# Performance work log

Measured on AMD Instinct MI355X. Metric: run time of the kernel, lower is better.

## Reference

```python
import jax, jax.numpy as jnp
import numpy as np

N_EMBD = 1024
N_HEAD = 16
B, T = 1, 4096
EPS = 1e-5


def layer_norm(x, w):
    mu = jnp.mean(x, axis=-1, keepdims=True)
    var = jnp.var(x, axis=-1, keepdims=True)
    return (x - mu) / jnp.sqrt(var + EPS) * w


def setup_inputs() -> dict:
    key = jax.random.key(0)
    ks = jax.random.split(key, 6)
    s = 0.02
    return {
        "x": jax.random.normal(ks[0], (B, T, N_EMBD), dtype=jnp.float32),
        "w_qkv": jax.random.normal(ks[1], (N_EMBD, 3 * N_EMBD), dtype=jnp.float32) * s,
        "w_attn_proj": jax.random.normal(ks[2], (N_EMBD, N_EMBD), dtype=jnp.float32) * s,
        "w_fc": jax.random.normal(ks[3], (N_EMBD, 4 * N_EMBD), dtype=jnp.float32) * s,
        "w_mlp_proj": jax.random.normal(ks[4], (4 * N_EMBD, N_EMBD), dtype=jnp.float32) * s,
        "ln1_w": jnp.ones((N_EMBD,), dtype=jnp.float32),
        "ln2_w": jnp.ones((N_EMBD,), dtype=jnp.float32),
    }


def reference(x, w_qkv, w_attn_proj, w_fc, w_mlp_proj, ln1_w, ln2_w):
    Bq, Tq, C = x.shape
    hs = C // N_HEAD

    # --- attention branch (pre-norm) ---
    h = layer_norm(x, ln1_w)
    qkv = h @ w_qkv  # [B,T,3C]
    q, k, v = jnp.split(qkv, 3, axis=-1)
    q = q.reshape(Bq, Tq, N_HEAD, hs).transpose(0, 2, 1, 3)  # [B,H,T,hs]
    k = k.reshape(Bq, Tq, N_HEAD, hs).transpose(0, 2, 1, 3)
    v = v.reshape(Bq, Tq, N_HEAD, hs).transpose(0, 2, 1, 3)

    scores = jnp.einsum("bhqd,bhkd->bhqk", q, k) * (1.0 / jnp.sqrt(jnp.float32(hs)))
    causal = jnp.tril(jnp.ones((Tq, Tq), dtype=bool))
    scores = jnp.where(causal, scores, -jnp.inf)
    weights = jax.nn.softmax(scores, axis=-1)  # dropout=0 -> identity
    out = jnp.einsum("bhqk,bhkd->bhqd", weights, v)
    out = out.transpose(0, 2, 1, 3).reshape(Bq, Tq, C)
    x = x + out @ w_attn_proj

    # --- MLP branch (pre-norm) ---
    h = layer_norm(x, ln2_w)
    h = jax.nn.gelu(h @ w_fc, approximate=False)  # nn.GELU default is exact
    x = x + h @ w_mlp_proj
    return x
```

## Files before the change

kernel.cpp:

```cpp
#include <hip/hip_runtime.h>
#include <cstdint>

typedef __attribute__((ext_vector_type(8))) short short8;
typedef __attribute__((ext_vector_type(4))) float f32x4;

__device__ __forceinline__ float b2f(unsigned short u) {
    return __uint_as_float(((unsigned int)u) << 16);
}
__device__ __forceinline__ unsigned short f2b(float f) {
    unsigned int u = __float_as_uint(f);
    u += 0x7FFFu + ((u >> 16) & 1u);
    return (unsigned short)(u >> 16);
}

__device__ __forceinline__ void gload_lds16(const unsigned short* g, unsigned short* l) {
    __builtin_amdgcn_global_load_lds(
        (const __attribute__((address_space(1))) uint32_t*)g,
        (__attribute__((address_space(3))) uint32_t*)l, 16, 0, 0);
}

__global__ __launch_bounds__(256) void k_transpose_bf16(
        const float* __restrict__ w, unsigned short* __restrict__ wT, int K, int N) {
    __shared__ float tile[32][33];
    int n0 = blockIdx.x * 32, k0 = blockIdx.y * 32;
    int tx = threadIdx.x, ty = threadIdx.y;
#pragma unroll
    for (int i = 0; i < 4; i++)
        tile[ty + 8 * i][tx] = w[(size_t)(k0 + ty + 8 * i) * N + n0 + tx];
    __syncthreads();
#pragma unroll
    for (int i = 0; i < 4; i++)
        wT[(size_t)(n0 + ty + 8 * i) * K + k0 + tx] = f2b(tile[tx][ty + 8 * i]);
}

__global__ __launch_bounds__(256) void k_layernorm(
        const float* __restrict__ x, const float* __restrict__ w,
        unsigned short* __restrict__ out) {
    int row = blockIdx.x, tid = threadIdx.x;
    const float4* xr = (const float4*)(x + (size_t)row * 1024);
    float4 v = xr[tid];
    float s  = v.x + v.y + v.z + v.w;
    float ss = v.x * v.x + v.y * v.y + v.z * v.z + v.w * v.w;
#pragma unroll
    for (int off = 32; off >= 1; off >>= 1) {
        s  += __shfl_down(s, off);
        ss += __shfl_down(ss, off);
    }
    __shared__ float red[10];
    if ((tid & 63) == 0) { red[tid >> 6] = s; red[4 + (tid >> 6)] = ss; }
    __syncthreads();
    if (tid == 0) {
        float S  = red[0] + red[1] + red[2] + red[3];
        float SS = red[4] + red[5] + red[6] + red[7];
        float mu  = S * (1.0f / 1024.0f);
        float var = SS * (1.0f / 1024.0f) - mu * mu;
        red[8] = mu; red[9] = rsqrtf(var + 1e-5f);
    }
    __syncthreads();
    float mu = red[8], rs = red[9];
    float4 wv = ((const float4*)w)[tid];
    ushort4 pk;
    pk.x = f2b((v.x - mu) * rs * wv.x);
    pk.y = f2b((v.y - mu) * rs * wv.y);
    pk.z = f2b((v.z - mu) * rs * wv.z);
    pk.w = f2b((v.w - mu) * rs * wv.w);
    *(ushort4*)(out + (size_t)row * 1024 + tid * 4) = pk;
}

template <int EPI, int TN>
__global__ __launch_bounds__(256) void k_gemm_bt(
        const unsigned short* __restrict__ A, const unsigned short* __restrict__ BT,
        const float* __restrict__ RES, void* __restrict__ OUT,
        int M, int N, int K) {
    constexpr int MI = (TN == 128) ? 4 : 2;
    __shared__ __align__(16) unsigned short As[128 * 64];
    __shared__ __align__(16) unsigned short Bs[TN * 64];
    int tid  = threadIdx.x;
    int lane = tid & 63, wave = tid >> 6;
    int quad = lane >> 4, qr = lane & 15;
    int wm_off = (TN == 128) ? (wave >> 1) * 64 : wave * 32;
    int wn_off = (TN == 128) ? (wave & 1) * 64 : 0;
    int m0 = blockIdx.y * 128, n0 = blockIdx.x * TN;
    int lrow = lane >> 3;
    int gcol = 8 * (((lane & 7) - lrow) & 7);
    int cswz[2];
#pragma unroll
    for (int kk = 0; kk < 2; kk++) cswz[kk] = 8 * (((kk * 4) + quad + (qr & 7)) & 7);
    f32x4 acc[MI][4] = {};
    for (int k0 = 0; k0 < K; k0 += 64) {
        __syncthreads();
#pragma unroll
        for (int t = 0; t < 4; t++) {
            int rowb = wave * 32 + t * 8;
            gload_lds16(&A[(size_t)(m0 + rowb + lrow) * K + k0 + gcol], &As[rowb * 64]);
        }
#pragma unroll
        for (int t = 0; t < TN / 32; t++) {
            int rowb = wave * (TN / 4) + t * 8;
            gload_lds16(&BT[(size_t)(n0 + rowb + lrow) * K + k0 + gcol], &Bs[rowb * 64]);
        }
        __syncthreads();
#pragma unroll
        for (int kk = 0; kk < 2; kk++) {
            short8 af[MI], bfr[4];
#pragma unroll
            for (int i = 0; i < MI; i++) af[i]  = *(const short8*)&As[(wm_off + i * 16 + qr) * 64 + cswz[kk]];
#pragma unroll
            for (int j = 0; j < 4; j++)  bfr[j] = *(const short8*)&Bs[(wn_off + j * 16 + qr) * 64 + cswz[kk]];
#pragma unroll
            for (int i = 0; i < MI; i++)
#pragma unroll
                for (int j = 0; j < 4; j++)
                    acc[i][j] = __builtin_amdgcn_mfma_f32_16x16x32_bf16(af[i], bfr[j], acc[i][j], 0, 0, 0);
        }
    }
#pragma unroll
    for (int i = 0; i < MI; i++) {
#pragma unroll
        for (int j = 0; j < 4; j++) {
#pragma unroll
            for (int r = 0; r < 4; r++) {
                int row = m0 + wm_off + i * 16 + quad * 4 + r;
                int col = n0 + wn_off + j * 16 + qr;
                size_t idx = (size_t)row * N + col;
                float v = acc[i][j][r];
                if (EPI == 0)      ((float*)OUT)[idx] = v;
                else if (EPI == 1) ((unsigned short*)OUT)[idx] = f2b(v);
                else if (EPI == 2) ((float*)OUT)[idx] = RES[idx] + v;
                else {
                    float u = v * fmaf(v * v, 0.035677408f, 0.79788456f);
                    float e = fminf(u * 2.885390082f, 80.0f);
                    float t = exp2f(e);
                    float g = v * t / (t + 1.0f);
                    ((unsigned short*)OUT)[idx] = f2b(g);
                }
            }
        }
    }
}

__global__ __launch_bounds__(256) void k_attn(
        const unsigned short* __restrict__ qkv, unsigned short* __restrict__ out) {
    __shared__ unsigned short Ks[128][72];
    __shared__ unsigned short Vt[64][136];
    __shared__ unsigned short Ps[4][16][136];

    const float C1 = 0.18033688f;
    const float C2 = 5.77078016f;

    int l = blockIdx.x;
    int h = l & 15;
    int qb = 63 - (l >> 4);
    int q0 = qb * 64;

    int tid = threadIdx.x;
    int wave = tid >> 6, lane = tid & 63;
    int lane16 = lane & 15, quad = lane >> 4;

    {
        int srow = tid >> 2, sc0 = (tid & 3) * 16;
        size_t base = (size_t)(q0 + srow) * 3072 + h * 64 + sc0;
        *(uint4*)&Ks[srow][sc0]     = *(const uint4*)&qkv[base];
        *(uint4*)&Ks[srow][sc0 + 8] = *(const uint4*)&qkv[base + 8];
    }
    __syncthreads();
    short8 aq0 = *(const short8*)&Ks[wave * 16 + lane16][quad * 8];
    short8 aq1 = *(const short8*)&Ks[wave * 16 + lane16][32 + quad * 8];

    f32x4 Oacc[4] = {};
    float l_part[4] = {0.f, 0.f, 0.f, 0.f};

    int vk = (lane & 31) * 2;
    int d0 = wave * 16 + (lane >> 5) * 8;

    for (int kc = 0; kc <= qb; kc += 2) {
        __syncthreads();
        {
            int srow = tid >> 1, c0 = (tid & 1) * 32;
            size_t base = (size_t)(kc * 64 + srow) * 3072 + 1024 + h * 64 + c0;
            *(uint4*)&Ks[srow][c0]      = *(const uint4*)&qkv[base];
            *(uint4*)&Ks[srow][c0 + 8]  = *(const uint4*)&qkv[base + 8];
            *(uint4*)&Ks[srow][c0 + 16] = *(const uint4*)&qkv[base + 16];
            *(uint4*)&Ks[srow][c0 + 24] = *(const uint4*)&qkv[base + 24];
        }
        {
#pragma unroll
            for (int c2 = 0; c2 < 2; c2++) {
                size_t vb = (size_t)((kc + c2) * 64 + vk) * 3072 + 2048 + h * 64 + d0;
                uint4 ve = *(const uint4*)&qkv[vb];
                uint4 vo = *(const uint4*)&qkv[vb + 3072];
                const unsigned short* pe = (const unsigned short*)&ve;
                const unsigned short* po = (const unsigned short*)&vo;
#pragma unroll
                for (int j = 0; j < 8; j++)
                    *(uint32_t*)&Vt[d0 + j][c2 * 64 + vk] =
                        (uint32_t)pe[j] | ((uint32_t)po[j] << 16);
            }
        }
        __syncthreads();

        f32x4 sacc[8] = {};
#pragma unroll
        for (int kt = 0; kt < 8; kt++) {
            short8 bk0 = *(const short8*)&Ks[kt * 16 + lane16][quad * 8];
            short8 bk1 = *(const short8*)&Ks[kt * 16 + lane16][32 + quad * 8];
            sacc[kt] = __builtin_amdgcn_mfma_f32_16x16x32_bf16(aq0, bk0, sacc[kt], 0, 0, 0);
            sacc[kt] = __builtin_amdgcn_mfma_f32_16x16x32_bf16(aq1, bk1, sacc[kt], 0, 0, 0);
        }

        bool domask = (kc + 2 > qb);
#pragma unroll
        for (int r = 0; r < 4; r++) {
            int qrow = q0 + wave * 16 + quad * 4 + r;
#pragma unroll
            for (int kt = 0; kt < 8; kt++) {
                float s = sacc[kt][r];
                if (domask) {
                    int key = kc * 64 + kt * 16 + lane16;
                    s = (key <= qrow) ? s : -__builtin_inff();
                }
                float p = exp2f(fmaf(s, C1, -C2));
                l_part[r] += p;
                Ps[wave][quad * 4 + r][kt * 16 + lane16] = f2b(p);
            }
        }
        __syncthreads();

#pragma unroll
        for (int s = 0; s < 4; s++) {
            short8 ap = *(const short8*)&Ps[wave][lane16][s * 32 + quad * 8];
#pragma unroll
            for (int dt = 0; dt < 4; dt++) {
                short8 bv = *(const short8*)&Vt[dt * 16 + lane16][s * 32 + quad * 8];
                Oacc[dt] = __builtin_amdgcn_mfma_f32_16x16x32_bf16(ap, bv, Oacc[dt], 0, 0, 0);
            }
        }
    }

    float invl[4];
#pragma unroll
    for (int r = 0; r < 4; r++) {
        float lf = l_part[r];
        lf += __shfl_xor(lf, 1);
        lf += __shfl_xor(lf, 2);
        lf += __shfl_xor(lf, 4);
        lf += __shfl_xor(lf, 8);
        invl[r] = 1.0f / lf;
    }
#pragma unroll
    for (int dt = 0; dt < 4; dt++) {
#pragma unroll
        for (int r = 0; r < 4; r++) {
            int qrow = q0 + wave * 16 + quad * 4 + r;
            out[(size_t)qrow * 1024 + h * 64 + dt * 16 + lane16] = f2b(Oacc[dt][r] * invl[r]);
        }
    }
}

extern "C" void kernel_launch(void* const* d_in, const int* in_sizes, int n_in,
                              void* d_out, int out_size, void* d_ws, size_t ws_size,
                              hipStream_t stream) {
    const float* x      = (const float*)d_in[0];
    const float* w_qkv  = (const float*)d_in[1];
    const float* w_attn = (const float*)d_in[2];
    const float* w_fc   = (const float*)d_in[3];
    const float* w_mlp  = (const float*)d_in[4];
    const float* ln1w   = (const float*)d_in[5];
    const float* ln2w   = (const float*)d_in[6];

    char* ws = (char*)d_ws;
    unsigned short* h      = (unsigned short*)(ws + 0);
    unsigned short* wqkvT  = (unsigned short*)(ws + 8388608);
    unsigned short* wattnT = (unsigned short*)(ws + 14680064);
    unsigned short* wfcT   = (unsigned short*)(ws + 16777216);
    unsigned short* wmlpT  = (unsigned short*)(ws + 25165824);
    unsigned short* qkv    = (unsigned short*)(ws + 33554432);
    unsigned short* attno  = (unsigned short*)(ws + 58720256);
    float*          x2     = (float*)(ws + 67108864);
    unsigned short* fcact  = (unsigned short*)(ws + 83886080);
    float* outF = (float*)d_out;

    dim3 tb(32, 8);
    k_transpose_bf16<<<dim3(96, 32),  tb, 0, stream>>>(w_qkv,  wqkvT,  1024, 3072);
    k_transpose_bf16<<<dim3(32, 32),  tb, 0, stream>>>(w_attn, wattnT, 1024, 1024);
    k_transpose_bf16<<<dim3(128, 32), tb, 0, stream>>>(w_fc,   wfcT,   1024, 4096);
    k_transpose_bf16<<<dim3(32, 128), tb, 0, stream>>>(w_mlp,  wmlpT,  4096, 1024);

    k_layernorm<<<4096, 256, 0, stream>>>(x, ln1w, h);
    k_gemm_bt<1, 128><<<dim3(24, 32), 256, 0, stream>>>(h, wqkvT, nullptr, qkv, 4096, 3072, 1024);
    k_attn<<<1024, 256, 0, stream>>>(qkv, attno);
    k_gemm_bt<2, 64><<<dim3(16, 32), 256, 0, stream>>>(attno, wattnT, x, x2, 4096, 1024, 1024);
    k_layernorm<<<4096, 256, 0, stream>>>(x2, ln2w, h);
    k_gemm_bt<3, 128><<<dim3(32, 32), 256, 0, stream>>>(h, wfcT, nullptr, fcact, 4096, 4096, 1024);
    k_gemm_bt<2, 64><<<dim3(16, 32), 256, 0, stream>>>(fcact, wmlpT, x2, outF, 4096, 1024, 4096);
}
```

Before: 426.1 us.

## Split-K with atomic residual accumulation for projection GEMMs; shuffle-pack P stores

The two N=1024 projection GEMMs now use 256x64 tiles with a split-K grid dimension. Each split accumulates into an output buffer that a copy kernel pre-fills with the residual, using float atomic adds. The attention kernel now packs pairs of P rows with lane shuffles so it can issue 32-bit LDS stores, and drops a barrier between the P write and the P·V matmul. This raises block count and wave utilization for the small-N GEMMs and cuts LDS store traffic, at the cost of extra copy kernels, atomic contention, and nondeterministic summation order.

```diff
diff --git a/kernel.cpp b/kernel.cpp
--- a/kernel.cpp
+++ b/kernel.cpp
@@ -17,6 +17,12 @@
     __builtin_amdgcn_global_load_lds(
         (const __attribute__((address_space(1))) uint32_t*)g,
         (__attribute__((address_space(3))) uint32_t*)l, 16, 0, 0);
+}
+
+__global__ __launch_bounds__(256) void k_copy(
+        const float* __restrict__ src, float* __restrict__ dst, int n4) {
+    int i = blockIdx.x * 256 + threadIdx.x;
+    if (i < n4) ((float4*)dst)[i] = ((const float4*)src)[i];
 }
 
 __global__ __launch_bounds__(256) void k_transpose_bf16(
@@ -67,31 +73,32 @@
     *(ushort4*)(out + (size_t)row * 1024 + tid * 4) = pk;
 }
 
-template <int EPI, int TN>
+template <int EPI, int TM, int TN>
 __global__ __launch_bounds__(256) void k_gemm_bt(
         const unsigned short* __restrict__ A, const unsigned short* __restrict__ BT,
         const float* __restrict__ RES, void* __restrict__ OUT,
         int M, int N, int K) {
-    constexpr int MI = (TN == 128) ? 4 : 2;
-    __shared__ __align__(16) unsigned short As[128 * 64];
+    __shared__ __align__(16) unsigned short As[TM * 64];
     __shared__ __align__(16) unsigned short Bs[TN * 64];
     int tid  = threadIdx.x;
     int lane = tid & 63, wave = tid >> 6;
     int quad = lane >> 4, qr = lane & 15;
-    int wm_off = (TN == 128) ? (wave >> 1) * 64 : wave * 32;
-    int wn_off = (TN == 128) ? (wave & 1) * 64 : 0;
-    int m0 = blockIdx.y * 128, n0 = blockIdx.x * TN;
+    int wm_off = (TM == 128) ? (wave >> 1) * 64 : wave * 64;
+    int wn_off = (TM == 128) ? (wave & 1) * 64 : 0;
+    int m0 = blockIdx.y * TM, n0 = blockIdx.x * TN;
+    int ks = K / gridDim.z;
+    int kbeg = blockIdx.z * ks, kend = kbeg + ks;
     int lrow = lane >> 3;
     int gcol = 8 * (((lane & 7) - lrow) & 7);
     int cswz[2];
 #pragma unroll
     for (int kk = 0; kk < 2; kk++) cswz[kk] = 8 * (((kk * 4) + quad + (qr & 7)) & 7);
-    f32x4 acc[MI][4] = {};
-    for (int k0 = 0; k0 < K; k0 += 64) {
+    f32x4 acc[4][4] = {};
+    for (int k0 = kbeg; k0 < kend; k0 += 64) {
         __syncthreads();
 #pragma unroll
-        for (int t = 0; t < 4; t++) {
-            int rowb = wave * 32 + t * 8;
+        for (int t = 0; t < TM / 32; t++) {
+            int rowb = wave * (TM / 4) + t * 8;
             gload_lds16(&A[(size_t)(m0 + rowb + lrow) * K + k0 + gcol], &As[rowb * 64]);
         }
 #pragma unroll
@@ -102,20 +109,20 @@
         __syncthreads();
 #pragma unroll
         for (int kk = 0; kk < 2; kk++) {
-            short8 af[MI], bfr[4];
-#pragma unroll
-            for (int i = 0; i < MI; i++) af[i]  = *(const short8*)&As[(wm_off + i * 16 + qr) * 64 + cswz[kk]];
+            short8 af[4], bfr[4];
+#pragma unroll
+            for (int i = 0; i < 4; i++) af[i]  = *(const short8*)&As[(wm_off + i * 16 + qr) * 64 + cswz[kk]];
 #pragma unroll
             for (int j = 0; j < 4; j++)  bfr[j] = *(const short8*)&Bs[(wn_off + j * 16 + qr) * 64 + cswz[kk]];
 #pragma unroll
-            for (int i = 0; i < MI; i++)
+            for (int i = 0; i < 4; i++)
 #pragma unroll
                 for (int j = 0; j < 4; j++)
                     acc[i][j] = __builtin_amdgcn_mfma_f32_16x16x32_bf16(af[i], bfr[j], acc[i][j], 0, 0, 0);
         }
     }
 #pragma unroll
-    for (int i = 0; i < MI; i++) {
+    for (int i = 0; i < 4; i++) {
 #pragma unroll
         for (int j = 0; j < 4; j++) {
 #pragma unroll
@@ -124,9 +131,9 @@
                 int col = n0 + wn_off + j * 16 + qr;
                 size_t idx = (size_t)row * N + col;
                 float v = acc[i][j][r];
-                if (EPI == 0)      ((float*)OUT)[idx] = v;
-                else if (EPI == 1) ((unsigned short*)OUT)[idx] = f2b(v);
+                if (EPI == 1)      ((unsigned short*)OUT)[idx] = f2b(v);
                 else if (EPI == 2) ((float*)OUT)[idx] = RES[idx] + v;
+                else if (EPI == 4) unsafeAtomicAdd(&((float*)OUT)[idx], v);
                 else {
                     float u = v * fmaf(v * v, 0.035677408f, 0.79788456f);
                     float e = fminf(u * 2.885390082f, 80.0f);
@@ -156,6 +163,7 @@
     int tid = threadIdx.x;
     int wave = tid >> 6, lane = tid & 63;
     int lane16 = lane & 15, quad = lane >> 4;
+    bool even = !(lane16 & 1);
 
     {
         int srow = tid >> 2, sc0 = (tid & 3) * 16;
@@ -210,21 +218,31 @@
 
         bool domask = (kc + 2 > qb);
 #pragma unroll
-        for (int r = 0; r < 4; r++) {
-            int qrow = q0 + wave * 16 + quad * 4 + r;
-#pragma unroll
-            for (int kt = 0; kt < 8; kt++) {
+        for (int kt = 0; kt < 8; kt++) {
+            uint32_t u[4];
+#pragma unroll
+            for (int r = 0; r < 4; r++) {
                 float s = sacc[kt][r];
                 if (domask) {
                     int key = kc * 64 + kt * 16 + lane16;
+                    int qrow = q0 + wave * 16 + quad * 4 + r;
                     s = (key <= qrow) ? s : -__builtin_inff();
                 }
                 float p = exp2f(fmaf(s, C1, -C2));
                 l_part[r] += p;
-                Ps[wave][quad * 4 + r][kt * 16 + lane16] = f2b(p);
+                u[r] = __float_as_uint(p);
             }
-        }
-        __syncthreads();
+            uint32_t t0 = __shfl_xor((int)(even ? u[2] : u[0]), 1);
+            uint32_t t1 = __shfl_xor((int)(even ? u[3] : u[1]), 1);
+            uint32_t lo0 = even ? u[0] : t0, hi0 = even ? t0 : u[2];
+            uint32_t lo1 = even ? u[1] : t1, hi1 = even ? t1 : u[3];
+            uint32_t w0 = (lo0 >> 16) | (hi0 & 0xFFFF0000u);
+            uint32_t w1 = (lo1 >> 16) | (hi1 & 0xFFFF0000u);
+            int rowb = quad * 4 + (even ? 0 : 2);
+            int colp = kt * 16 + (lane16 & ~1);
+            *(uint32_t*)&Ps[wave][rowb][colp]     = w0;
+            *(uint32_t*)&Ps[wave][rowb + 1][colp] = w1;
+        }
 
 #pragma unroll
         for (int s = 0; s < 4; s++) {
@@ -287,10 +305,12 @@
     k_transpose_bf16<<<dim3(32, 128), tb, 0, stream>>>(w_mlp,  wmlpT,  4096, 1024);
 
     k_layernorm<<<4096, 256, 0, stream>>>(x, ln1w, h);
-    k_gemm_bt<1, 128><<<dim3(24, 32), 256, 0, stream>>>(h, wqkvT, nullptr, qkv, 4096, 3072, 1024);
+    k_gemm_bt<1, 128, 128><<<dim3(24, 32), 256, 0, stream>>>(h, wqkvT, nullptr, qkv, 4096, 3072, 1024);
+    k_copy<<<4096, 256, 0, stream>>>(x, x2, 1048576);
     k_attn<<<1024, 256, 0, stream>>>(qkv, attno);
-    k_gemm_bt<2, 64><<<dim3(16, 32), 256, 0, stream>>>(attno, wattnT, x, x2, 4096, 1024, 1024);
+    k_gemm_bt<4, 256, 64><<<dim3(16, 16, 2), 256, 0, stream>>>(attno, wattnT, nullptr, x2, 4096, 1024, 1024);
     k_layernorm<<<4096, 256, 0, stream>>>(x2, ln2w, h);
-    k_gemm_bt<3, 128><<<dim3(32, 32), 256, 0, stream>>>(h, wfcT, nullptr, fcact, 4096, 4096, 1024);
-    k_gemm_bt<2, 64><<<dim3(16, 32), 256, 0, stream>>>(fcact, wmlpT, x2, outF, 4096, 1024, 4096);
-}
+    k_copy<<<4096, 256, 0, stream>>>(x2, outF, 1048576);
+    k_gemm_bt<3, 128, 128><<<dim3(32, 32), 256, 0, stream>>>(h, wfcT, nullptr, fcact, 4096, 4096, 1024);
+    k_gemm_bt<4, 256, 64><<<dim3(16, 16, 4), 256, 0, stream>>>(fcact, wmlpT, nullptr, outF, 4096, 1024, 4096);
+}
```

Result: slower. 481.4 us (+13.0%).

## Prefetch next K/V tiles into registers and drop redundant barrier in attention

Applied to the files above, without the earlier changes.

The attention kernel now loads the next pair of K and V tiles from global memory into registers while the current tile's QK and PV MFMAs run, then stores them to LDS at the top of the next iteration. This is meant to hide global load latency behind compute. The barrier between writing the per-wave P tile and reading it is removed, since each wave touches only its own slice. The unused fp32 epilogue branch of the GEMM is also removed. The prefetch registers raise VGPR pressure and may lower occupancy.

```diff
diff --git a/kernel.cpp b/kernel.cpp
--- a/kernel.cpp
+++ b/kernel.cpp
@@ -124,8 +124,7 @@
                 int col = n0 + wn_off + j * 16 + qr;
                 size_t idx = (size_t)row * N + col;
                 float v = acc[i][j][r];
-                if (EPI == 0)      ((float*)OUT)[idx] = v;
-                else if (EPI == 1) ((unsigned short*)OUT)[idx] = f2b(v);
+                if (EPI == 1)      ((unsigned short*)OUT)[idx] = f2b(v);
                 else if (EPI == 2) ((float*)OUT)[idx] = RES[idx] + v;
                 else {
                     float u = v * fmaf(v * v, 0.035677408f, 0.79788456f);
@@ -170,34 +169,59 @@
     f32x4 Oacc[4] = {};
     float l_part[4] = {0.f, 0.f, 0.f, 0.f};
 
+    int srow = tid >> 1, sc0 = (tid & 1) * 32;
     int vk = (lane & 31) * 2;
     int d0 = wave * 16 + (lane >> 5) * 8;
+
+    uint4 pk0, pk1, pk2, pk3, pv0, pv1, pv2, pv3;
+    {
+        size_t base = (size_t)srow * 3072 + 1024 + h * 64 + sc0;
+        pk0 = *(const uint4*)&qkv[base];
+        pk1 = *(const uint4*)&qkv[base + 8];
+        pk2 = *(const uint4*)&qkv[base + 16];
+        pk3 = *(const uint4*)&qkv[base + 24];
+        size_t vb0 = (size_t)vk * 3072 + 2048 + h * 64 + d0;
+        pv0 = *(const uint4*)&qkv[vb0];
+        pv1 = *(const uint4*)&qkv[vb0 + 3072];
+        size_t vb1 = (size_t)(64 + vk) * 3072 + 2048 + h * 64 + d0;
+        pv2 = *(const uint4*)&qkv[vb1];
+        pv3 = *(const uint4*)&qkv[vb1 + 3072];
+    }
 
     for (int kc = 0; kc <= qb; kc += 2) {
         __syncthreads();
         {
-            int srow = tid >> 1, c0 = (tid & 1) * 32;
-            size_t base = (size_t)(kc * 64 + srow) * 3072 + 1024 + h * 64 + c0;
-            *(uint4*)&Ks[srow][c0]      = *(const uint4*)&qkv[base];
-            *(uint4*)&Ks[srow][c0 + 8]  = *(const uint4*)&qkv[base + 8];
-            *(uint4*)&Ks[srow][c0 + 16] = *(const uint4*)&qkv[base + 16];
-            *(uint4*)&Ks[srow][c0 + 24] = *(const uint4*)&qkv[base + 24];
+            *(uint4*)&Ks[srow][sc0]      = pk0;
+            *(uint4*)&Ks[srow][sc0 + 8]  = pk1;
+            *(uint4*)&Ks[srow][sc0 + 16] = pk2;
+            *(uint4*)&Ks[srow][sc0 + 24] = pk3;
         }
         {
-#pragma unroll
-            for (int c2 = 0; c2 < 2; c2++) {
-                size_t vb = (size_t)((kc + c2) * 64 + vk) * 3072 + 2048 + h * 64 + d0;
-                uint4 ve = *(const uint4*)&qkv[vb];
-                uint4 vo = *(const uint4*)&qkv[vb + 3072];
-                const unsigned short* pe = (const unsigned short*)&ve;
-                const unsigned short* po = (const unsigned short*)&vo;
-#pragma unroll
-                for (int j = 0; j < 8; j++)
-                    *(uint32_t*)&Vt[d0 + j][c2 * 64 + vk] =
-                        (uint32_t)pe[j] | ((uint32_t)po[j] << 16);
+            const unsigned short* pe0 = (const unsigned short*)&pv0;
+            const unsigned short* po0 = (const unsigned short*)&pv1;
+            const unsigned short* pe1 = (const unsigned short*)&pv2;
+            const unsigned short* po1 = (const unsigned short*)&pv3;
+#pragma unroll
+            for (int j = 0; j < 8; j++) {
+                *(uint32_t*)&Vt[d0 + j][vk]      = (uint32_t)pe0[j] | ((uint32_t)po0[j] << 16);
+                *(uint32_t*)&Vt[d0 + j][64 + vk] = (uint32_t)pe1[j] | ((uint32_t)po1[j] << 16);
             }
         }
         __syncthreads();
+
+        if (kc + 2 <= qb) {
+            size_t base = (size_t)((kc + 2) * 64 + srow) * 3072 + 1024 + h * 64 + sc0;
+            pk0 = *(const uint4*)&qkv[base];
+            pk1 = *(const uint4*)&qkv[base + 8];
+            pk2 = *(const uint4*)&qkv[base + 16];
+            pk3 = *(const uint4*)&qkv[base + 24];
+            size_t vb0 = (size_t)((kc + 2) * 64 + vk) * 3072 + 2048 + h * 64 + d0;
+            pv0 = *(const uint4*)&qkv[vb0];
+            pv1 = *(const uint4*)&qkv[vb0 + 3072];
+            size_t vb1 = (size_t)((kc + 3) * 64 + vk) * 3072 + 2048 + h * 64 + d0;
+            pv2 = *(const uint4*)&qkv[vb1];
+            pv3 = *(const uint4*)&qkv[vb1 + 3072];
+        }
 
         f32x4 sacc[8] = {};
 #pragma unroll
@@ -224,7 +248,6 @@
                 Ps[wave][quad * 4 + r][kt * 16 + lane16] = f2b(p);
             }
         }
-        __syncthreads();
 
 #pragma unroll
         for (int s = 0; s < 4; s++) {
```

Result: faster. 373.2 us (-12.4%).
